# Optimization experiments

Hardware: AMD Instinct MI355X
Metric: run time of the kernel (lower is better)

Reference implementation:

```python
import jax, jax.numpy as jnp
import numpy as np

B, S, D = 8, 4096, 512      # batch, seq_len, input_dim
H = 2048                    # expert hidden dim
O = 512                     # expert_output_dim
E = 8                       # num_experts
TOP_K = 1


def setup_inputs() -> dict:
    key = jax.random.key(0)
    ks = jax.random.split(key, 8)
    sc = 0.02
    return {
        "x": jax.random.normal(ks[0], (B, S, D), dtype=jnp.float32),
        "Wr": jax.random.normal(ks[1], (D, E), dtype=jnp.float32) * sc,
        "br": jnp.zeros((E,), dtype=jnp.float32),
        "W1": jax.random.normal(ks[2], (E, D, H), dtype=jnp.float32) * sc,
        "b1": jnp.zeros((E, H), dtype=jnp.float32),
        "W2": jax.random.normal(ks[3], (E, H, O), dtype=jnp.float32) * sc,
        "b2": jnp.zeros((E, O), dtype=jnp.float32),
    }


def reference(x, Wr, br, W1, b1, W2, b2):
    b, s, d = x.shape
    xf = x.reshape(-1, d)                                   # [T, D]
    router_logits = xf @ Wr + br                            # [T, E]
    topk_logits, topk_idx = jax.lax.top_k(router_logits, TOP_K)  # [T, K]
    topk_gates = jax.nn.softmax(topk_logits, axis=1)        # [T, K] (ones for K=1)

    out = jnp.zeros((xf.shape[0], O), dtype=x.dtype)
    for k in range(TOP_K):
        idx_k = topk_idx[:, k]                              # [T]
        gate_k = topk_gates[:, k:k + 1]                     # [T, 1]
        # loop over the small fixed expert set; mask-combine per token
        for e in range(E):
            h = jax.nn.relu(xf @ W1[e] + b1[e])             # [T, H]
            oe = h @ W2[e] + b2[e]                          # [T, O]
            mask = (idx_k == e)[:, None]                    # [T, 1]
            out = out + jnp.where(mask, gate_k * oe, 0.0)
    return out.reshape(b, s, O)
```

## Files before the change

kernel.cpp:

```cpp
#include <hip/hip_runtime.h>
#include <stdint.h>

#define N_TOK 32768
#define D_IN  512
#define H_DIM 2048
#define O_DIM 512
#define N_EXP 8
#define NTILES 272
#define TPX    34

typedef __bf16 bf16x8 __attribute__((ext_vector_type(8)));
typedef float  f32x4  __attribute__((ext_vector_type(4)));
typedef unsigned int u32x4 __attribute__((ext_vector_type(4)));

struct alignas(8) us4 { unsigned short x, y, z, w; };

#define FENCE() asm volatile("" ::: "memory")
#define BAR()   do { FENCE(); __builtin_amdgcn_s_barrier(); FENCE(); } while (0)
#define WAITV0  asm volatile("s_waitcnt vmcnt(0)" ::: "memory")

__device__ __forceinline__ unsigned short f2bf(float f) {
  union { float f; unsigned u; } v; v.f = f;
  unsigned r = v.u + 0x7FFFu + ((v.u >> 16) & 1u);
  return (unsigned short)(r >> 16);
}

__device__ __forceinline__ void gll16(const void* src, void* lds_dst) {
  __builtin_amdgcn_global_load_lds(
      (const __attribute__((address_space(1))) void*)src,
      (__attribute__((address_space(3))) void*)lds_dst, 16, 0, 0);
}

__global__ void k_init(int* counts) {
  if (threadIdx.x < N_EXP) counts[threadIdx.x] = 0;
}

__global__ void k_transpose(const float* __restrict__ W, unsigned short* __restrict__ WT,
                            int R, int C) {
  __shared__ unsigned short tile[64][72];
  int e = blockIdx.y;
  const float* src = W + (size_t)e * R * C;
  unsigned short* dst = WT + (size_t)e * R * C;
  int tilesC = C >> 6;
  int tc = (blockIdx.x % tilesC) << 6;
  int tr = (blockIdx.x / tilesC) << 6;
  int tid = threadIdx.x;
  int rq = tid >> 4;
  int cq = tid & 15;
#pragma unroll
  for (int q = 0; q < 4; ++q) {
    int r = q * 16 + rq;
    float4 v = *(const float4*)(src + (size_t)(tr + r) * C + tc + cq * 4);
    us4 b;
    b.x = f2bf(v.x); b.y = f2bf(v.y); b.z = f2bf(v.z); b.w = f2bf(v.w);
    *(us4*)&tile[r][cq * 4] = b;
  }
  __syncthreads();
#pragma unroll
  for (int q = 0; q < 4; ++q) {
    int cc = q * 16 + rq;
    int rr = cq * 4;
    us4 o;
    o.x = tile[rr + 0][cc]; o.y = tile[rr + 1][cc];
    o.z = tile[rr + 2][cc]; o.w = tile[rr + 3][cc];
    *(us4*)(dst + (size_t)(tc + cc) * R + tr + rr) = o;
  }
}

__global__ void k_router(const float* __restrict__ x, const float* __restrict__ Wr,
                         const float* __restrict__ br, int* __restrict__ expert_id,
                         unsigned short* __restrict__ xbf) {
  int token = blockIdx.x * 4 + (threadIdx.x >> 6);
  int lane  = threadIdx.x & 63;
  const float* xr = x + (size_t)token * D_IN;
  float acc[N_EXP];
#pragma unroll
  for (int e = 0; e < N_EXP; ++e) acc[e] = 0.f;
#pragma unroll
  for (int j = 0; j < 2; ++j) {
    int i0 = lane * 8 + j * 4;
    float4 xv = *(const float4*)(xr + i0);
    us4 bb;
    bb.x = f2bf(xv.x); bb.y = f2bf(xv.y); bb.z = f2bf(xv.z); bb.w = f2bf(xv.w);
    *(us4*)(xbf + (size_t)token * D_IN + i0) = bb;
    float xs[4] = {xv.x, xv.y, xv.z, xv.w};
#pragma unroll
    for (int u = 0; u < 4; ++u) {
      const float4* wr = (const float4*)(Wr + (size_t)(i0 + u) * N_EXP);
      float4 w0 = wr[0], w1 = wr[1];
      acc[0] += xs[u] * w0.x; acc[1] += xs[u] * w0.y;
      acc[2] += xs[u] * w0.z; acc[3] += xs[u] * w0.w;
      acc[4] += xs[u] * w1.x; acc[5] += xs[u] * w1.y;
      acc[6] += xs[u] * w1.z; acc[7] += xs[u] * w1.w;
    }
  }
#pragma unroll
  for (int off = 32; off > 0; off >>= 1) {
#pragma unroll
    for (int e = 0; e < N_EXP; ++e) acc[e] += __shfl_xor(acc[e], off, 64);
  }
  if (lane == 0) {
    float best = acc[0] + br[0]; int bi = 0;
#pragma unroll
    for (int e = 1; e < N_EXP; ++e) {
      float v = acc[e] + br[e];
      if (v > best) { best = v; bi = e; }
    }
    expert_id[token] = bi;
  }
}

__global__ void k_count(const int* __restrict__ expert_id, int* __restrict__ counts) {
  __shared__ int lcnt[N_EXP];
  int tid = threadIdx.x;
  if (tid < N_EXP) lcnt[tid] = 0;
  __syncthreads();
  int e = expert_id[blockIdx.x * 1024 + tid];
  atomicAdd(&lcnt[e], 1);
  __syncthreads();
  if (tid < N_EXP) atomicAdd(&counts[tid], lcnt[tid]);
}

__global__ void k_scan(const int* __restrict__ counts, int* __restrict__ offsets,
                       int* __restrict__ cursor, int2* __restrict__ table) {
  int i = threadIdx.x;
  int s = 0, ts = 0, myexp = -1, myt = -1;
#pragma unroll
  for (int e = 0; e < N_EXP; ++e) {
    int c = counts[e];
    int tc = (c + 127) >> 7;
    if (i == e) { offsets[e] = s; cursor[e] = s; }
    if (i >= ts && i < ts + tc) { myexp = e; myt = i - ts; }
    s += c; ts += tc;
  }
  if (i < NTILES) table[i] = make_int2(myexp, myt);
}

__global__ void k_scatter(const int* __restrict__ expert_id, int* __restrict__ cursor,
                          int* __restrict__ idx_list) {
  __shared__ int lcnt[N_EXP], lbase[N_EXP];
  int tid = threadIdx.x;
  int i = blockIdx.x * 512 + tid;
  if (tid < N_EXP) lcnt[tid] = 0;
  __syncthreads();
  int e = expert_id[i];
  int lpos = atomicAdd(&lcnt[e], 1);
  __syncthreads();
  if (tid < N_EXP) lbase[tid] = atomicAdd(&cursor[tid], lcnt[tid]);
  __syncthreads();
  idx_list[lbase[e] + lpos] = i;
}


__launch_bounds__(256, 4)
__global__ void k_gemm1(const unsigned short* __restrict__ xbf,
                        const unsigned short* __restrict__ W1T,
                        const float* __restrict__ b1,
                        const int* __restrict__ counts, const int* __restrict__ offsets,
                        const int2* __restrict__ table, const int* __restrict__ idx_list,
                        unsigned short* __restrict__ Hperm,
                        int nt1, int ch, int hchunk) {
  int xcd = blockIdx.x & 7;
  int s   = blockIdx.x >> 3;
  int tile  = xcd * TPX + s / nt1;
  int ntile = s % nt1;
  int2 et = table[tile];
  int e = et.x;
  if (e < 0) return;
  int base   = offsets[e] + et.y * 128;
  int mvalid = min(128, counts[e] - et.y * 128);

  __shared__ __align__(16) unsigned char lds[32768];

  int tid = threadIdx.x, w = tid >> 6, lane = tid & 63;
  int l15 = lane & 15, l4 = lane >> 4;
  int wr = w >> 1, wc = w & 1;
  int n0 = ch * hchunk + ntile * 128;

  unsigned offA[4], offB[4];
#pragma unroll
  for (int q = 0; q < 4; ++q) {
    int d   = q * 4096 + w * 1024 + lane * 16;
    int row = d >> 7;
    int bs  = (d & 127) ^ ((row & 7) << 4);
    int tok = idx_list[base + min(row, mvalid - 1)];
    offA[q] = (unsigned)tok * (D_IN * 2) + bs;
    offB[q] = (unsigned)(e * H_DIM + n0 + row) * (D_IN * 2) + bs;
  }

  f32x4 acc[4][4];
#pragma unroll
  for (int a = 0; a < 4; ++a)
#pragma unroll
    for (int b = 0; b < 4; ++b) acc[a][b] = (f32x4){0.f, 0.f, 0.f, 0.f};

#define STAGE1(kstep) do {                                                   \
    unsigned kb = (unsigned)(kstep) * 128u;                                  \
    _Pragma("unroll")                                                        \
    for (int q = 0; q < 4; ++q) {                                            \
      gll16((const char*)xbf + offA[q] + kb, lds + q * 4096 + w * 1024);     \
      gll16((const char*)W1T + offB[q] + kb, lds + 16384 + q * 4096 + w * 1024); \
    }                                                                        \
  } while (0)

#define COMPUTE1() do {                                                      \
    const unsigned char* A = lds;                                            \
    const unsigned char* B = lds + 16384;                                    \
    __builtin_amdgcn_s_setprio(1);                                           \
    _Pragma("unroll")                                                        \
    for (int ks = 0; ks < 2; ++ks) {                                         \
      int kb = ks * 64 + l4 * 16;                                            \
      bf16x8 bfr[4];                                                         \
      _Pragma("unroll")                                                      \
      for (int nf = 0; nf < 4; ++nf) {                                       \
        int n = wc * 64 + nf * 16 + l15;                                     \
        bfr[nf] = *(const bf16x8*)(B + n * 128 + (kb ^ ((n & 7) << 4)));     \
      }                                                                      \
      _Pragma("unroll")                                                      \
      for (int mf = 0; mf < 4; ++mf) {                                       \
        int m = wr * 64 + mf * 16 + l15;                                     \
        bf16x8 af = *(const bf16x8*)(A + m * 128 + (kb ^ ((m & 7) << 4)));   \
        _Pragma("unroll")                                                    \
        for (int nf = 0; nf < 4; ++nf)                                       \
          acc[mf][nf] = __builtin_amdgcn_mfma_f32_16x16x32_bf16(af, bfr[nf], acc[mf][nf], 0, 0, 0); \
      }                                                                      \
    }                                                                        \
    __builtin_amdgcn_s_setprio(0);                                           \
  } while (0)

  const int NK = D_IN / 64;
  for (int t = 0; t < NK; ++t) {
    STAGE1(t);
    WAITV0;
    BAR();
    COMPUTE1();
    BAR();
  }

#pragma unroll
  for (int nf = 0; nf < 4; ++nf) {
    int col = wc * 64 + nf * 16 + l15;
    float bv = b1[(size_t)e * H_DIM + n0 + col];
#pragma unroll
    for (int mf = 0; mf < 4; ++mf) {
#pragma unroll
      for (int j = 0; j < 4; ++j) {
        int row = wr * 64 + mf * 16 + l4 * 4 + j;
        float v = fmaxf(acc[mf][nf][j] + bv, 0.f);
        *(unsigned short*)(lds + row * 256 + ((col * 2) ^ ((row & 7) << 4))) = f2bf(v);
      }
    }
  }
  BAR();
  {
    int row = tid >> 1;
    int seg = (tid & 1) * 128;
    if (row < mvalid) {
      int swz = (row & 7) << 4;
      char* gdst = (char*)Hperm + ((size_t)(base + row) * hchunk + ntile * 128) * 2 + seg;
      const unsigned char* lsrc = lds + row * 256;
#pragma unroll
      for (int i = 0; i < 8; ++i) {
        u32x4 v = *(const u32x4*)(lsrc + ((seg + i * 16) ^ swz));
        *(u32x4*)(gdst + i * 16) = v;
      }
    }
  }
#undef STAGE1
#undef COMPUTE1
}

__launch_bounds__(256, 4)
__global__ void k_gemm2(const unsigned short* __restrict__ Hperm,
                        const unsigned short* __restrict__ W2T,
                        const float* __restrict__ b2,
                        const int* __restrict__ counts, const int* __restrict__ offsets,
                        const int2* __restrict__ table, const int* __restrict__ idx_list,
                        float* __restrict__ out,
                        int ch, int hchunk, int accumulate) {
  int xcd = blockIdx.x & 7;
  int s   = blockIdx.x >> 3;
  int tile  = xcd * TPX + (s >> 2);
  int ntile = s & 3;
  int2 et = table[tile];
  int e = et.x;
  if (e < 0) return;
  int base   = offsets[e] + et.y * 128;
  int mvalid = min(128, counts[e] - et.y * 128);

  __shared__ __align__(16) unsigned char lds[32768];

  int tid = threadIdx.x, w = tid >> 6, lane = tid & 63;
  int l15 = lane & 15, l4 = lane >> 4;
  int wr = w >> 1, wc = w & 1;
  int o0 = ntile * 128;
  const unsigned hrow = (unsigned)hchunk * 2;

  unsigned offA[4], offB[4];
#pragma unroll
  for (int q = 0; q < 4; ++q) {
    int d   = q * 4096 + w * 1024 + lane * 16;
    int row = d >> 7;
    int bs  = (d & 127) ^ ((row & 7) << 4);
    offA[q] = (unsigned)min(base + row, N_TOK - 1) * hrow + bs;
    offB[q] = (unsigned)(e * O_DIM + o0 + row) * (H_DIM * 2) + (unsigned)ch * hchunk * 2 + bs;
  }

  f32x4 acc[4][4];
#pragma unroll
  for (int a = 0; a < 4; ++a)
#pragma unroll
    for (int b = 0; b < 4; ++b) acc[a][b] = (f32x4){0.f, 0.f, 0.f, 0.f};

#define STAGE2(kstep) do {                                                   \
    unsigned kb = (unsigned)(kstep) * 128u;                                  \
    _Pragma("unroll")                                                        \
    for (int q = 0; q < 4; ++q) {                                            \
      gll16((const char*)Hperm + offA[q] + kb, lds + q * 4096 + w * 1024);   \
      gll16((const char*)W2T   + offB[q] + kb, lds + 16384 + q * 4096 + w * 1024); \
    }                                                                        \
  } while (0)

#define COMPUTE2() do {                                                      \
    const unsigned char* A = lds;                                            \
    const unsigned char* B = lds + 16384;                                    \
    __builtin_amdgcn_s_setprio(1);                                           \
    _Pragma("unroll")                                                        \
    for (int ks = 0; ks < 2; ++ks) {                                         \
      int kb = ks * 64 + l4 * 16;                                            \
      bf16x8 bfr[4];                                                         \
      _Pragma("unroll")                                                      \
      for (int nf = 0; nf < 4; ++nf) {                                       \
        int n = wc * 64 + nf * 16 + l15;                                     \
        bfr[nf] = *(const bf16x8*)(B + n * 128 + (kb ^ ((n & 7) << 4)));     \
      }                                                                      \
      _Pragma("unroll")                                                      \
      for (int mf = 0; mf < 4; ++mf) {                                       \
        int m = wr * 64 + mf * 16 + l15;                                     \
        bf16x8 af = *(const bf16x8*)(A + m * 128 + (kb ^ ((m & 7) << 4)));   \
        _Pragma("unroll")                                                    \
        for (int nf = 0; nf < 4; ++nf)                                       \
          acc[mf][nf] = __builtin_amdgcn_mfma_f32_16x16x32_bf16(af, bfr[nf], acc[mf][nf], 0, 0, 0); \
      }                                                                      \
    }                                                                        \
    __builtin_amdgcn_s_setprio(0);                                           \
  } while (0)

  const int NK = hchunk / 64;
  for (int t = 0; t < NK; ++t) {
    STAGE2(t);
    WAITV0;
    BAR();
    COMPUTE2();
    BAR();
  }

#pragma unroll
  for (int nf = 0; nf < 4; ++nf) {
    int o = o0 + wc * 64 + nf * 16 + l15;
    float bv = b2[(size_t)e * O_DIM + o];
#pragma unroll
    for (int mf = 0; mf < 4; ++mf) {
#pragma unroll
      for (int j = 0; j < 4; ++j) {
        int row = wr * 64 + mf * 16 + l4 * 4 + j;
        if (row < mvalid) {
          int tok = idx_list[base + row];
          float* p = out + (size_t)tok * O_DIM + o;
          if (accumulate) *p = *p + acc[mf][nf][j];
          else            *p = acc[mf][nf][j] + bv;
        }
      }
    }
  }
#undef STAGE2
#undef COMPUTE2
}

extern "C" void kernel_launch(void* const* d_in, const int* in_sizes, int n_in,
                              void* d_out, int out_size, void* d_ws, size_t ws_size,
                              hipStream_t stream) {
  const float* x  = (const float*)d_in[0];
  const float* Wr = (const float*)d_in[1];
  const float* br = (const float*)d_in[2];
  const float* W1 = (const float*)d_in[3];
  const float* b1 = (const float*)d_in[4];
  const float* W2 = (const float*)d_in[5];
  const float* b2 = (const float*)d_in[6];
  float* out = (float*)d_out;

  char* ws = (char*)d_ws;
  int*  counts    = (int*)(ws + 0);
  int*  offsets   = (int*)(ws + 64);
  int*  cursor    = (int*)(ws + 128);
  int2* table     = (int2*)(ws + 256);
  int*  expert_id = (int*)(ws + 4096);
  int*  idx_list  = (int*)(ws + 4096 + N_TOK * 4);
  size_t off = 4096 + 2 * (size_t)N_TOK * 4;
  unsigned short* xbf = (unsigned short*)(ws + off);
  off += (size_t)N_TOK * D_IN * 2;
  unsigned short* W1T = (unsigned short*)(ws + off);
  off += (size_t)N_EXP * H_DIM * D_IN * 2;
  unsigned short* W2T = (unsigned short*)(ws + off);
  off += (size_t)N_EXP * H_DIM * O_DIM * 2;
  unsigned short* Hperm = (unsigned short*)(ws + off);

  int hchunk = 2048;
  while (hchunk > 256 && off + (size_t)N_TOK * hchunk * 2 > ws_size) hchunk >>= 1;
  int nch = H_DIM / hchunk;
  int nt1 = hchunk / 128;

  k_init<<<1, 64, 0, stream>>>(counts);
  k_transpose<<<dim3(256, N_EXP), 256, 0, stream>>>(W1, W1T, D_IN, H_DIM);
  k_transpose<<<dim3(256, N_EXP), 256, 0, stream>>>(W2, W2T, H_DIM, O_DIM);
  k_router<<<N_TOK / 4, 256, 0, stream>>>(x, Wr, br, expert_id, xbf);
  k_count<<<N_TOK / 1024, 1024, 0, stream>>>(expert_id, counts);
  k_scan<<<1, 512, 0, stream>>>(counts, offsets, cursor, table);
  k_scatter<<<N_TOK / 512, 512, 0, stream>>>(expert_id, cursor, idx_list);

  for (int ch = 0; ch < nch; ++ch) {
    k_gemm1<<<8 * TPX * nt1, 256, 0, stream>>>(xbf, W1T, b1, counts, offsets,
                                               table, idx_list, Hperm, nt1, ch, hchunk);
    k_gemm2<<<8 * TPX * 4, 256, 0, stream>>>(Hperm, W2T, b2, counts, offsets,
                                             table, idx_list, out, ch, hchunk, ch > 0);
  }
}
```

Measured before the change: 332.3 us.

## Widen GEMM block tiles from 128x128 to 128x256 in both expert kernels

Each workgroup in both grouped GEMMs now computes two 128-column N tiles, so one staged A tile in LDS is reused across twice as many MFMAs. This halves the number of blocks and the redundant reloads of gathered token rows. LDS per block grows to 48KB and the accumulator count doubles, so launch bounds drop to 3 waves per SIMD and occupancy may fall. The GEMM1 epilogue writes the two N halves out one after the other, reusing LDS with an extra barrier.

After: 469.8 us. 1.41x slower.

```diff
diff --git a/kernel.cpp b/kernel.cpp
--- a/kernel.cpp
+++ b/kernel.cpp
@@ -152,30 +152,30 @@
 }
 
 
-__launch_bounds__(256, 4)
+__launch_bounds__(256, 3)
 __global__ void k_gemm1(const unsigned short* __restrict__ xbf,
                         const unsigned short* __restrict__ W1T,
                         const float* __restrict__ b1,
                         const int* __restrict__ counts, const int* __restrict__ offsets,
                         const int2* __restrict__ table, const int* __restrict__ idx_list,
                         unsigned short* __restrict__ Hperm,
-                        int nt1, int ch, int hchunk) {
+                        int nt2, int ch, int hchunk) {
   int xcd = blockIdx.x & 7;
   int s   = blockIdx.x >> 3;
-  int tile  = xcd * TPX + s / nt1;
-  int ntile = s % nt1;
+  int tile = xcd * TPX + s / nt2;
+  int ntp  = s % nt2;
   int2 et = table[tile];
   int e = et.x;
   if (e < 0) return;
   int base   = offsets[e] + et.y * 128;
   int mvalid = min(128, counts[e] - et.y * 128);
 
-  __shared__ __align__(16) unsigned char lds[32768];
+  __shared__ __align__(16) unsigned char lds[49152];
 
   int tid = threadIdx.x, w = tid >> 6, lane = tid & 63;
   int l15 = lane & 15, l4 = lane >> 4;
   int wr = w >> 1, wc = w & 1;
-  int n0 = ch * hchunk + ntile * 128;
+  int n0 = ch * hchunk + ntp * 256;
 
   unsigned offA[4], offB[4];
 #pragma unroll
@@ -187,19 +187,25 @@
     offA[q] = (unsigned)tok * (D_IN * 2) + bs;
     offB[q] = (unsigned)(e * H_DIM + n0 + row) * (D_IN * 2) + bs;
   }
-
-  f32x4 acc[4][4];
-#pragma unroll
-  for (int a = 0; a < 4; ++a)
-#pragma unroll
-    for (int b = 0; b < 4; ++b) acc[a][b] = (f32x4){0.f, 0.f, 0.f, 0.f};
+  const unsigned BROW128 = 128u * (D_IN * 2);
+
+  f32x4 acc[2][4][4];
+#pragma unroll
+  for (int a = 0; a < 2; ++a)
+#pragma unroll
+    for (int b = 0; b < 4; ++b)
+#pragma unroll
+      for (int c = 0; c < 4; ++c) acc[a][b][c] = (f32x4){0.f, 0.f, 0.f, 0.f};
 
 #define STAGE1(kstep) do {                                                   \
     unsigned kb = (unsigned)(kstep) * 128u;                                  \
     _Pragma("unroll")                                                        \
-    for (int q = 0; q < 4; ++q) {                                            \
+    for (int q = 0; q < 4; ++q)                                              \
       gll16((const char*)xbf + offA[q] + kb, lds + q * 4096 + w * 1024);     \
-      gll16((const char*)W1T + offB[q] + kb, lds + 16384 + q * 4096 + w * 1024); \
+    _Pragma("unroll")                                                        \
+    for (int q = 0; q < 8; ++q) {                                            \
+      unsigned src = offB[q & 3] + ((q >= 4) ? BROW128 : 0u) + kb;           \
+      gll16((const char*)W1T + src, lds + 16384 + q * 4096 + w * 1024);      \
     }                                                                        \
   } while (0)
 
@@ -210,19 +216,23 @@
     _Pragma("unroll")                                                        \
     for (int ks = 0; ks < 2; ++ks) {                                         \
       int kb = ks * 64 + l4 * 16;                                            \
-      bf16x8 bfr[4];                                                         \
+      bf16x8 bfr[2][4];                                                      \
       _Pragma("unroll")                                                      \
-      for (int nf = 0; nf < 4; ++nf) {                                       \
-        int n = wc * 64 + nf * 16 + l15;                                     \
-        bfr[nf] = *(const bf16x8*)(B + n * 128 + (kb ^ ((n & 7) << 4)));     \
-      }                                                                      \
+      for (int nt = 0; nt < 2; ++nt)                                         \
+        _Pragma("unroll")                                                    \
+        for (int nf = 0; nf < 4; ++nf) {                                     \
+          int n = nt * 128 + wc * 64 + nf * 16 + l15;                        \
+          bfr[nt][nf] = *(const bf16x8*)(B + n * 128 + (kb ^ ((n & 7) << 4))); \
+        }                                                                    \
       _Pragma("unroll")                                                      \
       for (int mf = 0; mf < 4; ++mf) {                                       \
         int m = wr * 64 + mf * 16 + l15;                                     \
         bf16x8 af = *(const bf16x8*)(A + m * 128 + (kb ^ ((m & 7) << 4)));   \
         _Pragma("unroll")                                                    \
-        for (int nf = 0; nf < 4; ++nf)                                       \
-          acc[mf][nf] = __builtin_amdgcn_mfma_f32_16x16x32_bf16(af, bfr[nf], acc[mf][nf], 0, 0, 0); \
+        for (int nt = 0; nt < 2; ++nt)                                       \
+          _Pragma("unroll")                                                  \
+          for (int nf = 0; nf < 4; ++nf)                                     \
+            acc[nt][mf][nf] = __builtin_amdgcn_mfma_f32_16x16x32_bf16(af, bfr[nt][nf], acc[nt][mf][nf], 0, 0, 0); \
       }                                                                      \
     }                                                                        \
     __builtin_amdgcn_s_setprio(0);                                           \
@@ -237,40 +247,50 @@
     BAR();
   }
 
-#pragma unroll
-  for (int nf = 0; nf < 4; ++nf) {
-    int col = wc * 64 + nf * 16 + l15;
-    float bv = b1[(size_t)e * H_DIM + n0 + col];
-#pragma unroll
-    for (int mf = 0; mf < 4; ++mf) {
-#pragma unroll
-      for (int j = 0; j < 4; ++j) {
-        int row = wr * 64 + mf * 16 + l4 * 4 + j;
-        float v = fmaxf(acc[mf][nf][j] + bv, 0.f);
-        *(unsigned short*)(lds + row * 256 + ((col * 2) ^ ((row & 7) << 4))) = f2bf(v);
+  float bv[2][4];
+#pragma unroll
+  for (int nt = 0; nt < 2; ++nt)
+#pragma unroll
+    for (int nf = 0; nf < 4; ++nf)
+      bv[nt][nf] = b1[(size_t)e * H_DIM + n0 + nt * 128 + wc * 64 + nf * 16 + l15];
+
+#pragma unroll
+  for (int nt = 0; nt < 2; ++nt) {
+#pragma unroll
+    for (int nf = 0; nf < 4; ++nf) {
+      int col = wc * 64 + nf * 16 + l15;
+#pragma unroll
+      for (int mf = 0; mf < 4; ++mf) {
+#pragma unroll
+        for (int j = 0; j < 4; ++j) {
+          int row = wr * 64 + mf * 16 + l4 * 4 + j;
+          float v = fmaxf(acc[nt][mf][nf][j] + bv[nt][nf], 0.f);
+          *(unsigned short*)(lds + row * 256 + ((col * 2) ^ ((row & 7) << 4))) = f2bf(v);
+        }
       }
     }
-  }
-  BAR();
-  {
-    int row = tid >> 1;
-    int seg = (tid & 1) * 128;
-    if (row < mvalid) {
-      int swz = (row & 7) << 4;
-      char* gdst = (char*)Hperm + ((size_t)(base + row) * hchunk + ntile * 128) * 2 + seg;
-      const unsigned char* lsrc = lds + row * 256;
-#pragma unroll
-      for (int i = 0; i < 8; ++i) {
-        u32x4 v = *(const u32x4*)(lsrc + ((seg + i * 16) ^ swz));
-        *(u32x4*)(gdst + i * 16) = v;
+    BAR();
+    {
+      int row = tid >> 1;
+      int seg = (tid & 1) * 128;
+      if (row < mvalid) {
+        int swz = (row & 7) << 4;
+        char* gdst = (char*)Hperm + ((size_t)(base + row) * hchunk + ntp * 256 + nt * 128) * 2 + seg;
+        const unsigned char* lsrc = lds + row * 256;
+#pragma unroll
+        for (int i = 0; i < 8; ++i) {
+          u32x4 v = *(const u32x4*)(lsrc + ((seg + i * 16) ^ swz));
+          *(u32x4*)(gdst + i * 16) = v;
+        }
       }
     }
+    BAR();
   }
 #undef STAGE1
 #undef COMPUTE1
 }
 
-__launch_bounds__(256, 4)
+__launch_bounds__(256, 3)
 __global__ void k_gemm2(const unsigned short* __restrict__ Hperm,
                         const unsigned short* __restrict__ W2T,
                         const float* __restrict__ b2,
@@ -280,20 +300,20 @@
                         int ch, int hchunk, int accumulate) {
   int xcd = blockIdx.x & 7;
   int s   = blockIdx.x >> 3;
-  int tile  = xcd * TPX + (s >> 2);
-  int ntile = s & 3;
+  int tile = xcd * TPX + (s >> 1);
+  int ntp  = s & 1;
   int2 et = table[tile];
   int e = et.x;
   if (e < 0) return;
   int base   = offsets[e] + et.y * 128;
   int mvalid = min(128, counts[e] - et.y * 128);
 
-  __shared__ __align__(16) unsigned char lds[32768];
+  __shared__ __align__(16) unsigned char lds[49152];
 
   int tid = threadIdx.x, w = tid >> 6, lane = tid & 63;
   int l15 = lane & 15, l4 = lane >> 4;
   int wr = w >> 1, wc = w & 1;
-  int o0 = ntile * 128;
+  int o0 = ntp * 256;
   const unsigned hrow = (unsigned)hchunk * 2;
 
   unsigned offA[4], offB[4];
@@ -305,19 +325,25 @@
     offA[q] = (unsigned)min(base + row, N_TOK - 1) * hrow + bs;
     offB[q] = (unsigned)(e * O_DIM + o0 + row) * (H_DIM * 2) + (unsigned)ch * hchunk * 2 + bs;
   }
-
-  f32x4 acc[4][4];
-#pragma unroll
-  for (int a = 0; a < 4; ++a)
-#pragma unroll
-    for (int b = 0; b < 4; ++b) acc[a][b] = (f32x4){0.f, 0.f, 0.f, 0.f};
+  const unsigned BROW128 = 128u * (H_DIM * 2);
+
+  f32x4 acc[2][4][4];
+#pragma unroll
+  for (int a = 0; a < 2; ++a)
+#pragma unroll
+    for (int b = 0; b < 4; ++b)
+#pragma unroll
+      for (int c = 0; c < 4; ++c) acc[a][b][c] = (f32x4){0.f, 0.f, 0.f, 0.f};
 
 #define STAGE2(kstep) do {                                                   \
     unsigned kb = (unsigned)(kstep) * 128u;                                  \
     _Pragma("unroll")                                                        \
-    for (int q = 0; q < 4; ++q) {                                            \
+    for (int q = 0; q < 4; ++q)                                              \
       gll16((const char*)Hperm + offA[q] + kb, lds + q * 4096 + w * 1024);   \
-      gll16((const char*)W2T   + offB[q] + kb, lds + 16384 + q * 4096 + w * 1024); \
+    _Pragma("unroll")                                                        \
+    for (int q = 0; q < 8; ++q) {                                            \
+      unsigned src = offB[q & 3] + ((q >= 4) ? BROW128 : 0u) + kb;           \
+      gll16((const char*)W2T + src, lds + 16384 + q * 4096 + w * 1024);      \
     }                                                                        \
   } while (0)
 
@@ -328,19 +354,23 @@
     _Pragma("unroll")                                                        \
     for (int ks = 0; ks < 2; ++ks) {                                         \
       int kb = ks * 64 + l4 * 16;                                            \
-      bf16x8 bfr[4];                                                         \
+      bf16x8 bfr[2][4];                                                      \
       _Pragma("unroll")                                                      \
-      for (int nf = 0; nf < 4; ++nf) {                                       \
-        int n = wc * 64 + nf * 16 + l15;                                     \
-        bfr[nf] = *(const bf16x8*)(B + n * 128 + (kb ^ ((n & 7) << 4)));     \
-      }                                                                      \
+      for (int nt = 0; nt < 2; ++nt)                                         \
+        _Pragma("unroll")                                                    \
+        for (int nf = 0; nf < 4; ++nf) {                                     \
+          int n = nt * 128 + wc * 64 + nf * 16 + l15;                        \
+          bfr[nt][nf] = *(const bf16x8*)(B + n * 128 + (kb ^ ((n & 7) << 4))); \
+        }                                                                    \
       _Pragma("unroll")                                                      \
       for (int mf = 0; mf < 4; ++mf) {                                       \
         int m = wr * 64 + mf * 16 + l15;                                     \
         bf16x8 af = *(const bf16x8*)(A + m * 128 + (kb ^ ((m & 7) << 4)));   \
         _Pragma("unroll")                                                    \
-        for (int nf = 0; nf < 4; ++nf)                                       \
-          acc[mf][nf] = __builtin_amdgcn_mfma_f32_16x16x32_bf16(af, bfr[nf], acc[mf][nf], 0, 0, 0); \
+        for (int nt = 0; nt < 2; ++nt)                                       \
+          _Pragma("unroll")                                                  \
+          for (int nf = 0; nf < 4; ++nf)                                     \
+            acc[nt][mf][nf] = __builtin_amdgcn_mfma_f32_16x16x32_bf16(af, bfr[nt][nf], acc[nt][mf][nf], 0, 0, 0); \
       }                                                                      \
     }                                                                        \
     __builtin_amdgcn_s_setprio(0);                                           \
@@ -356,19 +386,22 @@
   }
 
 #pragma unroll
-  for (int nf = 0; nf < 4; ++nf) {
-    int o = o0 + wc * 64 + nf * 16 + l15;
-    float bv = b2[(size_t)e * O_DIM + o];
-#pragma unroll
-    for (int mf = 0; mf < 4; ++mf) {
-#pragma unroll
-      for (int j = 0; j < 4; ++j) {
-        int row = wr * 64 + mf * 16 + l4 * 4 + j;
-        if (row < mvalid) {
-          int tok = idx_list[base + row];
-          float* p = out + (size_t)tok * O_DIM + o;
-          if (accumulate) *p = *p + acc[mf][nf][j];
-          else            *p = acc[mf][nf][j] + bv;
+  for (int nt = 0; nt < 2; ++nt) {
+#pragma unroll
+    for (int nf = 0; nf < 4; ++nf) {
+      int o = o0 + nt * 128 + wc * 64 + nf * 16 + l15;
+      float bvv = b2[(size_t)e * O_DIM + o];
+#pragma unroll
+      for (int mf = 0; mf < 4; ++mf) {
+#pragma unroll
+        for (int j = 0; j < 4; ++j) {
+          int row = wr * 64 + mf * 16 + l4 * 4 + j;
+          if (row < mvalid) {
+            int tok = idx_list[base + row];
+            float* p = out + (size_t)tok * O_DIM + o;
+            if (accumulate) *p = *p + acc[nt][mf][nf][j];
+            else            *p = acc[nt][mf][nf][j] + bvv;
+          }
         }
       }
     }
@@ -408,7 +441,7 @@
   int hchunk = 2048;
   while (hchunk > 256 && off + (size_t)N_TOK * hchunk * 2 > ws_size) hchunk >>= 1;
   int nch = H_DIM / hchunk;
-  int nt1 = hchunk / 128;
+  int nt2 = hchunk / 256;
 
   k_init<<<1, 64, 0, stream>>>(counts);
   k_transpose<<<dim3(256, N_EXP), 256, 0, stream>>>(W1, W1T, D_IN, H_DIM);
@@ -419,9 +452,9 @@
   k_scatter<<<N_TOK / 512, 512, 0, stream>>>(expert_id, cursor, idx_list);
 
   for (int ch = 0; ch < nch; ++ch) {
-    k_gemm1<<<8 * TPX * nt1, 256, 0, stream>>>(xbf, W1T, b1, counts, offsets,
-                                               table, idx_list, Hperm, nt1, ch, hchunk);
-    k_gemm2<<<8 * TPX * 4, 256, 0, stream>>>(Hperm, W2T, b2, counts, offsets,
+    k_gemm1<<<8 * TPX * nt2, 256, 0, stream>>>(xbf, W1T, b1, counts, offsets,
+                                               table, idx_list, Hperm, nt2, ch, hchunk);
+    k_gemm2<<<8 * TPX * 2, 256, 0, stream>>>(Hperm, W2T, b2, counts, offsets,
                                              table, idx_list, out, ch, hchunk, ch > 0);
   }
 }
```
